# Kernel optimization log

Measured on AMD Instinct MI355X. Metric: run time of the kernel, lower is better.

The kernel has to match this reference:

```python
import jax, jax.numpy as jnp
import numpy as np

N = 50000          # nodes
E = 1_600_000      # edges (avg degree 32)
IN = 16            # in_node_features
H0 = 64            # hidden_features_mlp[0]
D = 32             # hidden_features_mlp[1] == hidden_features_gnn
HF = 64            # hidden_final
OUT = 3            # out_features (congestion classes)
L = 3              # gnn_layer_num
EPS = 1e-5


def gelu(x):
    return jax.nn.gelu(x, approximate=False)  # torch nn.GELU default (erf)


def bn_eval(x, g, b):
    # BatchNorm1d in eval mode with fresh running stats (mean=0, var=1)
    return x * (g / jnp.sqrt(1.0 + EPS)) + b


def ln(x, g, b):
    m = jnp.mean(x, axis=-1, keepdims=True)
    v = jnp.var(x, axis=-1, keepdims=True)
    return (x - m) / jnp.sqrt(v + EPS) * g + b


def setup_inputs() -> dict:
    key = jax.random.key(0)
    ks = jax.random.split(key, 24)
    s = 0.1
    inp = {
        "x": jax.random.normal(ks[0], (N, IN), dtype=jnp.float32),
        "edge_index": jax.random.randint(ks[1], (2, E), 0, N, dtype=jnp.int32),
        # node_emb_mlp
        "emb_W1": jax.random.normal(ks[2], (IN, H0), dtype=jnp.float32) * s,
        "emb_b1": jnp.zeros((H0,), jnp.float32),
        "emb_bn1_g": jnp.ones((H0,), jnp.float32),
        "emb_bn1_b": jnp.zeros((H0,), jnp.float32),
        "emb_W2": jax.random.normal(ks[3], (H0, D), dtype=jnp.float32) * s,
        "emb_b2": jnp.zeros((D,), jnp.float32),
        "emb_bn2_g": jnp.ones((D,), jnp.float32),
        "emb_bn2_b": jnp.zeros((D,), jnp.float32),
        # GNN layers (stacked over L)
        "msg_W": jax.random.normal(ks[4], (L, 2 * D, D), dtype=jnp.float32) * s,
        "msg_b": jnp.zeros((L, D), jnp.float32),
        "msg_ln_g": jnp.ones((L, D), jnp.float32),
        "msg_ln_b": jnp.zeros((L, D), jnp.float32),
        "upd_W": jax.random.normal(ks[5], (L, 2 * D, D), dtype=jnp.float32) * s,
        "upd_b": jnp.zeros((L, D), jnp.float32),
        "upd_ln_g": jnp.ones((L, D), jnp.float32),
        "upd_ln_b": jnp.zeros((L, D), jnp.float32),
        # final_aggregation_layer
        "fin_W1": jax.random.normal(ks[6], (D, HF), dtype=jnp.float32) * s,
        "fin_b1": jnp.zeros((HF,), jnp.float32),
        "fin_bn_g": jnp.ones((HF,), jnp.float32),
        "fin_bn_b": jnp.zeros((HF,), jnp.float32),
        "fin_W2": jax.random.normal(ks[7], (HF, OUT), dtype=jnp.float32) * s,
        "fin_b2": jnp.zeros((OUT,), jnp.float32),
    }
    return inp


def reference(x, edge_index,
              emb_W1, emb_b1, emb_bn1_g, emb_bn1_b,
              emb_W2, emb_b2, emb_bn2_g, emb_bn2_b,
              msg_W, msg_b, msg_ln_g, msg_ln_b,
              upd_W, upd_b, upd_ln_g, upd_ln_b,
              fin_W1, fin_b1, fin_bn_g, fin_bn_b, fin_W2, fin_b2):
    src = edge_index[0]  # x_j (source, messages flow source->target)
    dst = edge_index[1]  # x_i (target, aggregation index)

    # node embedding MLP (dropout = identity in eval)
    h = gelu(bn_eval(x @ emb_W1 + emb_b1, emb_bn1_g, emb_bn1_b))
    h = gelu(bn_eval(h @ emb_W2 + emb_b2, emb_bn2_g, emb_bn2_b))
    pre = h

    for l in range(L):
        x_i = h[dst]  # [E, D]
        x_j = h[src]  # [E, D]
        m = gelu(ln(jnp.concatenate([x_i, x_j], axis=-1) @ msg_W[l] + msg_b[l],
                    msg_ln_g[l], msg_ln_b[l]))                 # [E, D]
        agg = jax.ops.segment_sum(m, dst, num_segments=N)      # [N, D]
        h = h + gelu(ln(jnp.concatenate([h, agg], axis=-1) @ upd_W[l] + upd_b[l],
                        upd_ln_g[l], upd_ln_b[l]))

    h = h + pre  # residual around the GNN stack

    general_emb = h[dst] - h[src]  # node_emb_j - node_emb_i, [E, D]
    out = gelu(bn_eval(general_emb @ fin_W1 + fin_b1, fin_bn_g, fin_bn_b))
    out = out @ fin_W2 + fin_b2  # [E, OUT] cc_scores
    return out
```

## Files before the change

kernel.cpp:

```cpp
#include <hip/hip_runtime.h>

#define NN 50000
#define NE 1600000
#define FILL_B 1563
#define EMB_B  782
#define HIST_STRIDE 100096
constexpr float LN_EPS = 1e-5f;

typedef _Float16 half8 __attribute__((ext_vector_type(8)));

__device__ __forceinline__ float gelu_f(float x){
  float ax = fabsf(x) * 0.70710678118654752440f;
  float t  = __builtin_amdgcn_rcpf(fmaf(0.3275911f, ax, 1.0f));
  float e  = __expf(-ax*ax);
  float p  = t*fmaf(t, fmaf(t, fmaf(t, fmaf(t, 1.061405429f, -1.453152027f),
                                    1.421413741f), -0.284496736f), 0.254829592f);
  float er = fmaf(-p, e, 1.0f);
  return 0.5f * x * (1.0f + copysignf(er, x));
}

__device__ __forceinline__ void ld8(const float* __restrict__ p, float* r){
  float4 a=((const float4*)p)[0], b=((const float4*)p)[1];
  r[0]=a.x;r[1]=a.y;r[2]=a.z;r[3]=a.w;r[4]=b.x;r[5]=b.y;r[6]=b.z;r[7]=b.w;
}
__device__ __forceinline__ void ld16(const float* __restrict__ p, float* r){ ld8(p,r); ld8(p+8,r+8); }
__device__ __forceinline__ void st8(float* __restrict__ p, const float* r){
  float4 a,b; a.x=r[0];a.y=r[1];a.z=r[2];a.w=r[3]; b.x=r[4];b.y=r[5];b.z=r[6];b.w=r[7];
  ((float4*)p)[0]=a; ((float4*)p)[1]=b;
}

__global__ __launch_bounds__(256) void hist_kernel(const int* __restrict__ ei,
    int* __restrict__ cnt16, int* __restrict__ rank){
  int t = blockIdx.x*256 + threadIdx.x;
  int hi = (blockIdx.x & 15) << 20;
  int* mycnt = cnt16 + (size_t)(blockIdx.x & 15)*NN;
  int i0 = t, i1 = t + HIST_STRIDE, i2 = t + 2*HIST_STRIDE, i3 = t + 3*HIST_STRIDE;
  bool v0 = i0 < NE/4, v1 = i1 < NE/4, v2 = i2 < NE/4, v3 = i3 < NE/4;
  int4 d0 = v0 ? ((const int4*)(ei + NE))[i0] : make_int4(0,0,0,0);
  int4 d1 = v1 ? ((const int4*)(ei + NE))[i1] : make_int4(0,0,0,0);
  int4 d2 = v2 ? ((const int4*)(ei + NE))[i2] : make_int4(0,0,0,0);
  int4 d3 = v3 ? ((const int4*)(ei + NE))[i3] : make_int4(0,0,0,0);
  int4 r0, r1, r2, r3;
  if(v0){ r0.x = hi|atomicAdd(&mycnt[d0.x],1); r0.y = hi|atomicAdd(&mycnt[d0.y],1);
          r0.z = hi|atomicAdd(&mycnt[d0.z],1); r0.w = hi|atomicAdd(&mycnt[d0.w],1); }
  if(v1){ r1.x = hi|atomicAdd(&mycnt[d1.x],1); r1.y = hi|atomicAdd(&mycnt[d1.y],1);
          r1.z = hi|atomicAdd(&mycnt[d1.z],1); r1.w = hi|atomicAdd(&mycnt[d1.w],1); }
  if(v2){ r2.x = hi|atomicAdd(&mycnt[d2.x],1); r2.y = hi|atomicAdd(&mycnt[d2.y],1);
          r2.z = hi|atomicAdd(&mycnt[d2.z],1); r2.w = hi|atomicAdd(&mycnt[d2.w],1); }
  if(v3){ r3.x = hi|atomicAdd(&mycnt[d3.x],1); r3.y = hi|atomicAdd(&mycnt[d3.y],1);
          r3.z = hi|atomicAdd(&mycnt[d3.z],1); r3.w = hi|atomicAdd(&mycnt[d3.w],1); }
  if(v0) ((int4*)rank)[i0] = r0;
  if(v1) ((int4*)rank)[i1] = r1;
  if(v2) ((int4*)rank)[i2] = r2;
  if(v3) ((int4*)rank)[i3] = r3;
}

__global__ __launch_bounds__(256) void reduce16_kernel(int* __restrict__ cnt16,
    int* __restrict__ deg){
  int n = blockIdx.x*256 + threadIdx.x;
  if(n >= NN) return;
  int run = 0;
  #pragma unroll
  for(int x=0;x<16;x++){
    int c = cnt16[(size_t)x*NN + n];
    cnt16[(size_t)x*NN + n] = run;
    run += c;
  }
  deg[n] = run;
}

#define CHUNK 52
__global__ __launch_bounds__(1024) void scan_kernel(const int* __restrict__ deg, int* __restrict__ row_ptr){
  __shared__ int sums[1024];
  int t = threadIdx.x;
  int base = t*CHUNK;
  int4 v[13];
  int ssum = 0;
  #pragma unroll
  for(int i=0;i<13;i++){
    int idx = base + 4*i;
    if(idx + 3 < NN){
      v[i] = ((const int4*)deg)[(base>>2)+i];
    } else {
      v[i].x = (idx+0<NN)?deg[idx+0]:0; v[i].y = (idx+1<NN)?deg[idx+1]:0;
      v[i].z = (idx+2<NN)?deg[idx+2]:0; v[i].w = (idx+3<NN)?deg[idx+3]:0;
    }
    ssum += v[i].x + v[i].y + v[i].z + v[i].w;
  }
  sums[t]=ssum;
  __syncthreads();
  for(int off=1; off<1024; off<<=1){
    int vv = (t>=off) ? sums[t-off] : 0;
    __syncthreads();
    sums[t] += vv;
    __syncthreads();
  }
  int run = (t>0) ? sums[t-1] : 0;
  #pragma unroll
  for(int i=0;i<13;i++){
    int idx = base + 4*i;
    int4 o;
    o.x = run; run += v[i].x;
    o.y = run; run += v[i].y;
    o.z = run; run += v[i].z;
    o.w = run; run += v[i].w;
    if(idx + 3 < NN){
      ((int4*)row_ptr)[(base>>2)+i] = o;
    } else {
      if(idx+0<NN) row_ptr[idx+0]=o.x;
      if(idx+1<NN) row_ptr[idx+1]=o.y;
      if(idx+2<NN) row_ptr[idx+2]=o.z;
      if(idx+3<NN) row_ptr[idx+3]=o.w;
    }
  }
  if(t==1023) row_ptr[NN] = sums[1023];
}

__global__ __launch_bounds__(256) void addbase16_kernel(int* __restrict__ cnt16,
    const int* __restrict__ row_ptr){
  int t = blockIdx.x*256 + threadIdx.x;
  if(t >= 16*(NN/4)) return;
  int x  = t / (NN/4);
  int n4 = t - x*(NN/4);
  int4 rp = ((const int4*)row_ptr)[n4];
  int4 c  = ((int4*)(cnt16 + (size_t)x*NN))[n4];
  c.x += rp.x; c.y += rp.y; c.z += rp.z; c.w += rp.w;
  ((int4*)(cnt16 + (size_t)x*NN))[n4] = c;
}

__global__ __launch_bounds__(256) void fill_embed_kernel(
    const int* __restrict__ ei,
    const int* __restrict__ rank, const int* __restrict__ base16,
    int* __restrict__ csr,
    const float* __restrict__ x,
    const float* __restrict__ W1, const float* __restrict__ b1,
    const float* __restrict__ g1, const float* __restrict__ bb1,
    const float* __restrict__ W2, const float* __restrict__ b2,
    const float* __restrict__ g2, const float* __restrict__ bb2,
    const float* __restrict__ Wm, const float* __restrict__ bm,
    const float* __restrict__ Wu, const float* __restrict__ bu,
    const float* __restrict__ fb1, const float* __restrict__ fbng, const float* __restrict__ fbnb,
    float* __restrict__ h, float* __restrict__ pre,
    float* __restrict__ P, _Float16* __restrict__ Qh, float* __restrict__ R,
    float* __restrict__ cvec)
{
  if(blockIdx.x >= EMB_B){
    int t = (blockIdx.x - EMB_B)*256 + threadIdx.x;
    if(t < NE/4){
      int4 d  = ((const int4*)(ei + NE))[t];
      int4 sv = ((const int4*)ei)[t];
      int4 rk = ((const int4*)rank)[t];
      csr[base16[(size_t)((unsigned)rk.x>>20)*NN + d.x] + (rk.x & 0xFFFFF)] = sv.x;
      csr[base16[(size_t)((unsigned)rk.y>>20)*NN + d.y] + (rk.y & 0xFFFFF)] = sv.y;
      csr[base16[(size_t)((unsigned)rk.z>>20)*NN + d.z] + (rk.z & 0xFFFFF)] = sv.z;
      csr[base16[(size_t)((unsigned)rk.w>>20)*NN + d.w] + (rk.w & 0xFFFFF)] = sv.w;
    }
    return;
  }
  int t = blockIdx.x*256 + threadIdx.x;
  const float rs = rsqrtf(1.0f + LN_EPS);
  if(t < 64) cvec[t] = fmaf(fb1[t], fbng[t]*rs, fbnb[t]);
  int n = t >> 2, q = t & 3;
  if(n >= NN) return;
  int base = threadIdx.x & 60;
  float4 xq = ((const float4*)x)[n*4 + q];
  float xv[16];
  #pragma unroll
  for(int m=0;m<4;m++){
    xv[4*m+0]=__shfl(xq.x, base|m);
    xv[4*m+1]=__shfl(xq.y, base|m);
    xv[4*m+2]=__shfl(xq.z, base|m);
    xv[4*m+3]=__shfl(xq.w, base|m);
  }
  float a1q[16]; ld16(b1 + q*16, a1q);
  #pragma unroll
  for(int k=0;k<16;k++){
    float w[16]; ld16(W1 + k*64 + q*16, w);
    float xk = xv[k];
    #pragma unroll
    for(int j=0;j<16;j++) a1q[j] += xk * w[j];
  }
  { float g[16], b[16]; ld16(g1+q*16,g); ld16(bb1+q*16,b);
    #pragma unroll
    for(int j=0;j<16;j++) a1q[j] = gelu_f(a1q[j]*(g[j]*rs) + b[j]); }
  float hq[8]; ld8(b2 + q*8, hq);
  #pragma unroll
  for(int m=0;m<4;m++){
    #pragma unroll
    for(int kk=0;kk<16;kk++){
      float a = __shfl(a1q[kk], base|m);
      float w[8]; ld8(W2 + (m*16+kk)*32 + q*8, w);
      #pragma unroll
      for(int j=0;j<8;j++) hq[j] += a * w[j];
    }
  }
  { float g[8], b[8]; ld8(g2+q*8,g); ld8(bb2+q*8,b);
    #pragma unroll
    for(int j=0;j<8;j++) hq[j] = gelu_f(hq[j]*(g[j]*rs) + b[j]); }
  st8(h   + (size_t)n*32 + q*8, hq);
  st8(pre + (size_t)n*32 + q*8, hq);
  float apv[8], aqv[8], arv[8];
  ld8(bm+q*8, apv); ld8(bu+q*8, arv);
  #pragma unroll
  for(int j=0;j<8;j++) aqv[j]=0.f;
  #pragma unroll
  for(int m=0;m<4;m++){
    #pragma unroll
    for(int kk=0;kk<8;kk++){
      float hk = __shfl(hq[kk], base|m);
      int k = m*8+kk;
      float wm[8],wq[8],wu[8];
      ld8(Wm + k*32      + q*8, wm);
      ld8(Wm + (32+k)*32 + q*8, wq);
      ld8(Wu + k*32      + q*8, wu);
      #pragma unroll
      for(int j=0;j<8;j++){ apv[j]+=hk*wm[j]; aqv[j]+=hk*wq[j]; arv[j]+=hk*wu[j]; }
    }
  }
  st8(P + (size_t)n*32 + q*8, apv);
  st8(R + (size_t)n*32 + q*8, arv);
  half8 qo;
  #pragma unroll
  for(int k=0;k<8;k++) qo[k] = (_Float16)aqv[k];
  *(half8*)(Qh + (size_t)n*32 + q*8) = qo;
}

__global__ __launch_bounds__(256) void msg_kernel(
    const float* __restrict__ P, const _Float16* __restrict__ Qh,
    const int* __restrict__ row_ptr, const int* __restrict__ csr_src,
    const float* __restrict__ mg, const float* __restrict__ mb,
    float* __restrict__ aggO)
{
  int tid = blockIdx.x*256 + threadIdx.x;
  int n = tid >> 5;
  int s = tid & 31;
  int slot = s >> 2;
  int q = s & 3;
  float mgq[8], mbq[8], p8[8];
  ld8(mg + q*8, mgq); ld8(mb + q*8, mbq);
  ld8(P + (size_t)n*32 + q*8, p8);
  float agg8[8] = {0,0,0,0,0,0,0,0};
  int e0 = row_ptr[n], e1 = row_ptr[n+1];
  int e  = e0 + slot;
  int e2 = e + 8;
  int src  = (e  < e1) ? csr_src[e]  : 0;
  int src2 = (e2 < e1) ? csr_src[e2] : 0;
  half8 qv = *(const half8*)(Qh + (size_t)src*32 + q*8);
  while(e < e1){
    half8 qv2 = *(const half8*)(Qh + (size_t)src2*32 + q*8);
    int e3 = e2 + 8;
    int src3 = (e3 < e1) ? csr_src[e3] : 0;
    float v[8];
    #pragma unroll
    for(int k=0;k<8;k++) v[k] = p8[k] + (float)qv[k];
    float ps = ((v[0]+v[1])+(v[2]+v[3])) + ((v[4]+v[5])+(v[6]+v[7]));
    ps += __shfl_xor(ps,1); ps += __shfl_xor(ps,2);
    float mean = ps * 0.03125f;
    float vs = 0.f;
    #pragma unroll
    for(int k=0;k<8;k++){ float dd = v[k]-mean; vs += dd*dd; v[k]=dd; }
    vs += __shfl_xor(vs,1); vs += __shfl_xor(vs,2);
    float rstd = rsqrtf(vs*0.03125f + LN_EPS);
    #pragma unroll
    for(int k=0;k<8;k++) agg8[k] += gelu_f(v[k]*rstd*mgq[k] + mbq[k]);
    qv = qv2; src2 = src3; e = e2; e2 = e3;
  }
  #pragma unroll
  for(int k=0;k<8;k++) agg8[k] += __shfl_xor(agg8[k], 4);
  #pragma unroll
  for(int k=0;k<8;k++) agg8[k] += __shfl_xor(agg8[k], 8);
  #pragma unroll
  for(int k=0;k<8;k++) agg8[k] += __shfl_xor(agg8[k], 16);
  if(slot==0) st8(aggO + (size_t)n*32 + q*8, agg8);
}

__global__ __launch_bounds__(256) void upd_pqr_kernel(
    const float* __restrict__ aggI, const float* __restrict__ Rio,
    const float* __restrict__ Ub,
    const float* __restrict__ ug, const float* __restrict__ ub,
    const float* __restrict__ Wm2, const float* __restrict__ bm2,
    const float* __restrict__ Wu2, const float* __restrict__ bu2,
    float* __restrict__ h,
    float* __restrict__ P, _Float16* __restrict__ Qh, float* __restrict__ Rout)
{
  int t = blockIdx.x*256 + threadIdx.x;
  int n = t >> 2, q = t & 3;
  if(n >= NN) return;
  int base = threadIdx.x & 60;
  float aggq[8], uq[8];
  ld8(aggI + (size_t)n*32 + q*8, aggq);
  ld8(Rio  + (size_t)n*32 + q*8, uq);
  #pragma unroll
  for(int m=0;m<4;m++){
    #pragma unroll
    for(int kk=0;kk<8;kk++){
      float a = __shfl(aggq[kk], base|m);
      float w[8]; ld8(Ub + (m*8+kk)*32 + q*8, w);
      #pragma unroll
      for(int j=0;j<8;j++) uq[j] += a * w[j];
    }
  }
  float sm = ((uq[0]+uq[1])+(uq[2]+uq[3])) + ((uq[4]+uq[5])+(uq[6]+uq[7]));
  sm += __shfl_xor(sm,1); sm += __shfl_xor(sm,2);
  float mean = sm * 0.03125f;
  float vs = 0.f;
  #pragma unroll
  for(int j=0;j<8;j++){ float d = uq[j]-mean; vs += d*d; uq[j]=d; }
  vs += __shfl_xor(vs,1); vs += __shfl_xor(vs,2);
  float rstd = rsqrtf(vs*0.03125f + LN_EPS);
  float ugq[8], ubq[8], hq[8];
  ld8(ug+q*8, ugq); ld8(ub+q*8, ubq);
  ld8(h + (size_t)n*32 + q*8, hq);
  #pragma unroll
  for(int j=0;j<8;j++) hq[j] += gelu_f(uq[j]*rstd*ugq[j] + ubq[j]);
  st8(h + (size_t)n*32 + q*8, hq);
  float apv[8], aqv[8], arv[8];
  ld8(bm2+q*8, apv); ld8(bu2+q*8, arv);
  #pragma unroll
  for(int j=0;j<8;j++) aqv[j]=0.f;
  #pragma unroll
  for(int m=0;m<4;m++){
    #pragma unroll
    for(int kk=0;kk<8;kk++){
      float hk = __shfl(hq[kk], base|m);
      int k = m*8+kk;
      float wm[8],wq[8],wu[8];
      ld8(Wm2 + k*32      + q*8, wm);
      ld8(Wm2 + (32+k)*32 + q*8, wq);
      ld8(Wu2 + k*32      + q*8, wu);
      #pragma unroll
      for(int j=0;j<8;j++){ apv[j]+=hk*wm[j]; aqv[j]+=hk*wq[j]; arv[j]+=hk*wu[j]; }
    }
  }
  st8(P    + (size_t)n*32 + q*8, apv);
  st8(Rout + (size_t)n*32 + q*8, arv);
  half8 qo;
  #pragma unroll
  for(int k=0;k<8;k++) qo[k] = (_Float16)aqv[k];
  *(half8*)(Qh + (size_t)n*32 + q*8) = qo;
}

__global__ __launch_bounds__(256) void upd_fin_kernel(
    const float* __restrict__ aggI, const float* __restrict__ Rio,
    const float* __restrict__ Ub,
    const float* __restrict__ ug, const float* __restrict__ ub,
    const float* __restrict__ h, const float* __restrict__ pre,
    const float* __restrict__ fW1, const float* __restrict__ fbng,
    _Float16* __restrict__ y1, _Float16* __restrict__ y2)
{
  int t = blockIdx.x*256 + threadIdx.x;
  int n = t >> 2, q = t & 3;
  if(n >= NN) return;
  int base = threadIdx.x & 60;
  const float rs = rsqrtf(1.0f + LN_EPS);
  float aggq[8], uq[8];
  ld8(aggI + (size_t)n*32 + q*8, aggq);
  ld8(Rio  + (size_t)n*32 + q*8, uq);
  #pragma unroll
  for(int m=0;m<4;m++){
    #pragma unroll
    for(int kk=0;kk<8;kk++){
      float a = __shfl(aggq[kk], base|m);
      float w[8]; ld8(Ub + (m*8+kk)*32 + q*8, w);
      #pragma unroll
      for(int j=0;j<8;j++) uq[j] += a * w[j];
    }
  }
  float sm = ((uq[0]+uq[1])+(uq[2]+uq[3])) + ((uq[4]+uq[5])+(uq[6]+uq[7]));
  sm += __shfl_xor(sm,1); sm += __shfl_xor(sm,2);
  float mean = sm * 0.03125f;
  float vs = 0.f;
  #pragma unroll
  for(int j=0;j<8;j++){ float d = uq[j]-mean; vs += d*d; uq[j]=d; }
  vs += __shfl_xor(vs,1); vs += __shfl_xor(vs,2);
  float rstd = rsqrtf(vs*0.03125f + LN_EPS);
  float ugq[8], ubq[8], hq[8], pq[8];
  ld8(ug+q*8, ugq); ld8(ub+q*8, ubq);
  ld8(h   + (size_t)n*32 + q*8, hq);
  ld8(pre + (size_t)n*32 + q*8, pq);
  #pragma unroll
  for(int j=0;j<8;j++) hq[j] += gelu_f(uq[j]*rstd*ugq[j] + ubq[j]) + pq[j];
  float acc[16];
  #pragma unroll
  for(int j=0;j<16;j++) acc[j]=0.f;
  #pragma unroll
  for(int m=0;m<4;m++){
    #pragma unroll
    for(int kk=0;kk<8;kk++){
      float hk = __shfl(hq[kk], base|m);
      float w[16]; ld16(fW1 + (m*8+kk)*64 + q*16, w);
      #pragma unroll
      for(int j=0;j<16;j++) acc[j] += hk * w[j];
    }
  }
  float fg[16]; ld16(fbng + q*16, fg);
  half8 o0, o1;
  #pragma unroll
  for(int k=0;k<8;k++){
    o0[k] = (_Float16)(acc[k]   * (fg[k]*rs));
    o1[k] = (_Float16)(acc[8+k] * (fg[8+k]*rs));
  }
  _Float16* dst = (q<2) ? (y1 + (size_t)n*32 + q*16) : (y2 + (size_t)n*32 + (q-2)*16);
  ((half8*)dst)[0] = o0; ((half8*)dst)[1] = o1;
}

__global__ __launch_bounds__(256) void finalA_kernel(
    const _Float16* __restrict__ y, const int* __restrict__ ei,
    const float* __restrict__ cvec, const float* __restrict__ W2,
    const float* __restrict__ b2, float* __restrict__ out)
{
  int t = blockIdx.x*256 + threadIdx.x;
  int g = t >> 2, q = t & 3;
  int eA = g, eB = g + NE/2;
  int sA = __builtin_nontemporal_load(ei + eA);
  int dA = __builtin_nontemporal_load(ei + NE + eA);
  int sB = __builtin_nontemporal_load(ei + eB);
  int dB = __builtin_nontemporal_load(ei + NE + eB);
  half8 aA = *(const half8*)(y + (size_t)dA*32 + q*8);
  half8 cA = *(const half8*)(y + (size_t)sA*32 + q*8);
  half8 aB = *(const half8*)(y + (size_t)dB*32 + q*8);
  half8 cB = *(const half8*)(y + (size_t)sB*32 + q*8);
  float cq[8]; ld8(cvec + q*8, cq);
  float w[24]; ld8(W2+q*24, w); ld8(W2+q*24+8, w+8); ld8(W2+q*24+16, w+16);
  float oA0=0.f,oA1=0.f,oA2=0.f, oB0=0.f,oB1=0.f,oB2=0.f;
  #pragma unroll
  for(int k=0;k<8;k++){
    float tA = gelu_f(((float)aA[k]-(float)cA[k]) + cq[k]);
    float tB = gelu_f(((float)aB[k]-(float)cB[k]) + cq[k]);
    oA0 += tA*w[3*k]; oA1 += tA*w[3*k+1]; oA2 += tA*w[3*k+2];
    oB0 += tB*w[3*k]; oB1 += tB*w[3*k+1]; oB2 += tB*w[3*k+2];
  }
  oA0 += __shfl_xor(oA0,1); oA0 += __shfl_xor(oA0,2);
  oA1 += __shfl_xor(oA1,1); oA1 += __shfl_xor(oA1,2);
  oA2 += __shfl_xor(oA2,1); oA2 += __shfl_xor(oA2,2);
  oB0 += __shfl_xor(oB0,1); oB0 += __shfl_xor(oB0,2);
  oB1 += __shfl_xor(oB1,1); oB1 += __shfl_xor(oB1,2);
  oB2 += __shfl_xor(oB2,1); oB2 += __shfl_xor(oB2,2);
  float ovA = (q==0) ? oA0 + b2[0] : (q==1) ? oA1 + b2[1] : oA2 + b2[2];
  float ovB = (q==0) ? oB0 + b2[0] : (q==1) ? oB1 + b2[1] : oB2 + b2[2];
  if(q < 3){
    __builtin_nontemporal_store(ovA, out + (size_t)eA*3 + q);
    __builtin_nontemporal_store(ovB, out + (size_t)eB*3 + q);
  }
}

__global__ __launch_bounds__(256) void finalB_kernel(
    const _Float16* __restrict__ y, const int* __restrict__ ei,
    const float* __restrict__ cvec, const float* __restrict__ W2,
    float* __restrict__ out)
{
  int t = blockIdx.x*256 + threadIdx.x;
  int g = t >> 2, q = t & 3;
  int eA = g, eB = g + NE/2;
  float pA = 0.f, pB = 0.f;
  if(q < 3){
    pA = __builtin_nontemporal_load(out + (size_t)eA*3 + q);
    pB = __builtin_nontemporal_load(out + (size_t)eB*3 + q);
  }
  int sA = __builtin_nontemporal_load(ei + eA);
  int dA = __builtin_nontemporal_load(ei + NE + eA);
  int sB = __builtin_nontemporal_load(ei + eB);
  int dB = __builtin_nontemporal_load(ei + NE + eB);
  half8 aA = *(const half8*)(y + (size_t)dA*32 + q*8);
  half8 cA = *(const half8*)(y + (size_t)sA*32 + q*8);
  half8 aB = *(const half8*)(y + (size_t)dB*32 + q*8);
  half8 cB = *(const half8*)(y + (size_t)sB*32 + q*8);
  float cq[8]; ld8(cvec + q*8, cq);
  float w[24]; ld8(W2+q*24, w); ld8(W2+q*24+8, w+8); ld8(W2+q*24+16, w+16);
  float oA0=0.f,oA1=0.f,oA2=0.f, oB0=0.f,oB1=0.f,oB2=0.f;
  #pragma unroll
  for(int k=0;k<8;k++){
    float tA = gelu_f(((float)aA[k]-(float)cA[k]) + cq[k]);
    float tB = gelu_f(((float)aB[k]-(float)cB[k]) + cq[k]);
    oA0 += tA*w[3*k]; oA1 += tA*w[3*k+1]; oA2 += tA*w[3*k+2];
    oB0 += tB*w[3*k]; oB1 += tB*w[3*k+1]; oB2 += tB*w[3*k+2];
  }
  oA0 += __shfl_xor(oA0,1); oA0 += __shfl_xor(oA0,2);
  oA1 += __shfl_xor(oA1,1); oA1 += __shfl_xor(oA1,2);
  oA2 += __shfl_xor(oA2,1); oA2 += __shfl_xor(oA2,2);
  oB0 += __shfl_xor(oB0,1); oB0 += __shfl_xor(oB0,2);
  oB1 += __shfl_xor(oB1,1); oB1 += __shfl_xor(oB1,2);
  oB2 += __shfl_xor(oB2,1); oB2 += __shfl_xor(oB2,2);
  float ovA = pA + ((q==0) ? oA0 : (q==1) ? oA1 : oA2);
  float ovB = pB + ((q==0) ? oB0 : (q==1) ? oB1 : oB2);
  if(q < 3){
    __builtin_nontemporal_store(ovA, out + (size_t)eA*3 + q);
    __builtin_nontemporal_store(ovB, out + (size_t)eB*3 + q);
  }
}

extern "C" void kernel_launch(void* const* d_in, const int* in_sizes, int n_in,
                              void* d_out, int out_size, void* d_ws, size_t ws_size,
                              hipStream_t stream)
{
  (void)in_sizes; (void)n_in; (void)out_size; (void)ws_size;
  const float* x     = (const float*)d_in[0];
  const int*   ei    = (const int*)d_in[1];
  const float* eW1   = (const float*)d_in[2];
  const float* eb1   = (const float*)d_in[3];
  const float* ebn1g = (const float*)d_in[4];
  const float* ebn1b = (const float*)d_in[5];
  const float* eW2   = (const float*)d_in[6];
  const float* eb2   = (const float*)d_in[7];
  const float* ebn2g = (const float*)d_in[8];
  const float* ebn2b = (const float*)d_in[9];
  const float* msgW  = (const float*)d_in[10];
  const float* msgb  = (const float*)d_in[11];
  const float* msglng= (const float*)d_in[12];
  const float* msglnb= (const float*)d_in[13];
  const float* updW  = (const float*)d_in[14];
  const float* updb  = (const float*)d_in[15];
  const float* updlng= (const float*)d_in[16];
  const float* updlnb= (const float*)d_in[17];
  const float* fW1   = (const float*)d_in[18];
  const float* fb1   = (const float*)d_in[19];
  const float* fbng  = (const float*)d_in[20];
  const float* fbnb  = (const float*)d_in[21];
  const float* fW2   = (const float*)d_in[22];
  const float* fb2   = (const float*)d_in[23];
  float* out = (float*)d_out;

  float* f   = (float*)d_ws;
  float* h   = f;
  float* pre = f + 1*(size_t)NN*32;
  float* P   = f + 2*(size_t)NN*32;
  float* R   = f + 3*(size_t)NN*32;
  float* agg = f + 4*(size_t)NN*32;
  _Float16* Qh = (_Float16*)(f + 5*(size_t)NN*32);
  _Float16* y1 = (_Float16*)P;
  _Float16* y2 = y1 + (size_t)NN*32;
  float* cvec  = f + 5*(size_t)NN*32 + (size_t)NN*16;
  int* ip      = (int*)(cvec + 64);
  int* cnt16   = ip;
  int* deg     = ip + 16*NN;
  int* row_ptr = ip + 17*NN;
  int* csr     = ip + 18*NN + 4;
  int* rank    = (int*)agg;

  hipMemsetAsync(cnt16, 0, (size_t)16*NN*sizeof(int), stream);
  hist_kernel<<<391, 256, 0, stream>>>(ei, cnt16, rank);
  reduce16_kernel<<<(NN+255)/256, 256, 0, stream>>>(cnt16, deg);
  scan_kernel<<<1, 1024, 0, stream>>>(deg, row_ptr);
  addbase16_kernel<<<(16*(NN/4)+255)/256, 256, 0, stream>>>(cnt16, row_ptr);
  fill_embed_kernel<<<EMB_B + FILL_B, 256, 0, stream>>>(ei, rank, cnt16, csr,
      x, eW1, eb1, ebn1g, ebn1b,
      eW2, eb2, ebn2g, ebn2b,
      msgW, msgb, updW, updb,
      fb1, fbng, fbnb,
      h, pre, P, Qh, R, cvec);

  for(int l=0; l<3; l++){
    msg_kernel<<<(NN*32)/256, 256, 0, stream>>>(P, Qh, row_ptr, csr,
        msglng + l*32, msglnb + l*32, agg);
    if(l < 2){
      upd_pqr_kernel<<<EMB_B, 256, 0, stream>>>(agg, R,
          updW + l*2048 + 1024, updlng + l*32, updlnb + l*32,
          msgW + (l+1)*2048, msgb + (l+1)*32,
          updW + (l+1)*2048, updb + (l+1)*32,
          h, P, Qh, R);
    } else {
      upd_fin_kernel<<<EMB_B, 256, 0, stream>>>(agg, R,
          updW + l*2048 + 1024, updlng + l*32, updlnb + l*32,
          h, pre, fW1, fbng, y1, y2);
    }
  }

  finalA_kernel<<<(NE*2)/256, 256, 0, stream>>>(y1, ei, cvec,      fW2,      fb2, out);
  finalB_kernel<<<(NE*2)/256, 256, 0, stream>>>(y2, ei, cvec + 32, fW2 + 96, out);
}
```

Baseline: 492.2 us.

## Assign one edge per lane in msg kernel with recursive-halving lane reduction

The message kernel is reorganized so that each lane processes a whole edge (all 32 features) rather than splitting an edge across 4 lanes with 8 edges in flight. This removes the per-edge shuffles for the LayerNorm mean and variance and replaces the final 24-shuffle reduction with a recursive-halving transpose reduction, so each lane writes one output feature. In exchange, register pressure rises sharply (roughly 128+ floats per thread). With degree about 32, many lanes sit idle on low-degree nodes, and the software prefetch of the next source index is dropped.

```diff
diff --git a/kernel.cpp b/kernel.cpp
--- a/kernel.cpp
+++ b/kernel.cpp
@@ -233,45 +233,81 @@
 {
   int tid = blockIdx.x*256 + threadIdx.x;
   int n = tid >> 5;
-  int s = tid & 31;
-  int slot = s >> 2;
-  int q = s & 3;
-  float mgq[8], mbq[8], p8[8];
-  ld8(mg + q*8, mgq); ld8(mb + q*8, mbq);
-  ld8(P + (size_t)n*32 + q*8, p8);
-  float agg8[8] = {0,0,0,0,0,0,0,0};
+  int lane = tid & 31;
+  float mgv[32], mbv[32], p[32];
+  ld16(mg, mgv); ld16(mg+16, mgv+16);
+  ld16(mb, mbv); ld16(mb+16, mbv+16);
+  ld16(P + (size_t)n*32, p); ld16(P + (size_t)n*32 + 16, p+16);
+  float agg[32];
+  #pragma unroll
+  for(int j=0;j<32;j++) agg[j]=0.f;
   int e0 = row_ptr[n], e1 = row_ptr[n+1];
-  int e  = e0 + slot;
-  int e2 = e + 8;
-  int src  = (e  < e1) ? csr_src[e]  : 0;
-  int src2 = (e2 < e1) ? csr_src[e2] : 0;
-  half8 qv = *(const half8*)(Qh + (size_t)src*32 + q*8);
-  while(e < e1){
-    half8 qv2 = *(const half8*)(Qh + (size_t)src2*32 + q*8);
-    int e3 = e2 + 8;
-    int src3 = (e3 < e1) ? csr_src[e3] : 0;
-    float v[8];
-    #pragma unroll
-    for(int k=0;k<8;k++) v[k] = p8[k] + (float)qv[k];
-    float ps = ((v[0]+v[1])+(v[2]+v[3])) + ((v[4]+v[5])+(v[6]+v[7]));
-    ps += __shfl_xor(ps,1); ps += __shfl_xor(ps,2);
-    float mean = ps * 0.03125f;
-    float vs = 0.f;
-    #pragma unroll
-    for(int k=0;k<8;k++){ float dd = v[k]-mean; vs += dd*dd; v[k]=dd; }
-    vs += __shfl_xor(vs,1); vs += __shfl_xor(vs,2);
-    float rstd = rsqrtf(vs*0.03125f + LN_EPS);
-    #pragma unroll
-    for(int k=0;k<8;k++) agg8[k] += gelu_f(v[k]*rstd*mgq[k] + mbq[k]);
-    qv = qv2; src2 = src3; e = e2; e2 = e3;
-  }
-  #pragma unroll
-  for(int k=0;k<8;k++) agg8[k] += __shfl_xor(agg8[k], 4);
-  #pragma unroll
-  for(int k=0;k<8;k++) agg8[k] += __shfl_xor(agg8[k], 8);
-  #pragma unroll
-  for(int k=0;k<8;k++) agg8[k] += __shfl_xor(agg8[k], 16);
-  if(slot==0) st8(aggO + (size_t)n*32 + q*8, agg8);
+  for(int e = e0 + lane; e < e1; e += 32){
+    int src = csr_src[e];
+    const half8* q4 = (const half8*)(Qh + (size_t)src*32);
+    half8 q0=q4[0], q1=q4[1], q2=q4[2], q3=q4[3];
+    float v[32];
+    #pragma unroll
+    for(int k=0;k<8;k++){
+      v[k]    = p[k]    + (float)q0[k];
+      v[8+k]  = p[8+k]  + (float)q1[k];
+      v[16+k] = p[16+k] + (float)q2[k];
+      v[24+k] = p[24+k] + (float)q3[k];
+    }
+    float s0=0,s1=0,s2=0,s3=0;
+    #pragma unroll
+    for(int i=0;i<8;i++){ s0+=v[4*i]; s1+=v[4*i+1]; s2+=v[4*i+2]; s3+=v[4*i+3]; }
+    float mean = ((s0+s1)+(s2+s3)) * 0.03125f;
+    s0=s1=s2=s3=0.f;
+    #pragma unroll
+    for(int i=0;i<8;i++){
+      float d0=v[4*i]-mean, d1=v[4*i+1]-mean, d2=v[4*i+2]-mean, d3=v[4*i+3]-mean;
+      s0+=d0*d0; s1+=d1*d1; s2+=d2*d2; s3+=d3*d3;
+      v[4*i]=d0; v[4*i+1]=d1; v[4*i+2]=d2; v[4*i+3]=d3;
+    }
+    float rstd = rsqrtf(((s0+s1)+(s2+s3))*0.03125f + LN_EPS);
+    #pragma unroll
+    for(int j=0;j<32;j++) agg[j] += gelu_f(v[j]*rstd*mgv[j] + mbv[j]);
+  }
+  float r16[16];
+  { int up = lane & 16;
+    #pragma unroll
+    for(int j=0;j<16;j++){
+      float mine   = up ? agg[16+j] : agg[j];
+      float theirs = up ? agg[j]    : agg[16+j];
+      r16[j] = mine + __shfl_xor(theirs, 16);
+    } }
+  float r8[8];
+  { int up = lane & 8;
+    #pragma unroll
+    for(int j=0;j<8;j++){
+      float mine   = up ? r16[8+j] : r16[j];
+      float theirs = up ? r16[j]   : r16[8+j];
+      r8[j] = mine + __shfl_xor(theirs, 8);
+    } }
+  float r4[4];
+  { int up = lane & 4;
+    #pragma unroll
+    for(int j=0;j<4;j++){
+      float mine   = up ? r8[4+j] : r8[j];
+      float theirs = up ? r8[j]   : r8[4+j];
+      r4[j] = mine + __shfl_xor(theirs, 4);
+    } }
+  float r2[2];
+  { int up = lane & 2;
+    #pragma unroll
+    for(int j=0;j<2;j++){
+      float mine   = up ? r4[2+j] : r4[j];
+      float theirs = up ? r4[j]   : r4[2+j];
+      r2[j] = mine + __shfl_xor(theirs, 2);
+    } }
+  float r1;
+  { int up = lane & 1;
+    float mine   = up ? r2[1] : r2[0];
+    float theirs = up ? r2[0] : r2[1];
+    r1 = mine + __shfl_xor(theirs, 1);
+  }
+  aggO[(size_t)n*32 + lane] = r1;
 }
 
 __global__ __launch_bounds__(256) void upd_pqr_kernel(
```

Measured after the change: 569.0 us. +15.6%, slower.
